# Performance work log

Hardware: AMD Instinct MI355X
Metric: run time of the kernel (lower is better)

## Reference

```python
import jax, jax.numpy as jnp
import numpy as np

B, S, F, D, H, L, NSUB, DFF = 64, 128, 62, 256, 4, 6, 32, 512
DH = D // 2           # each attention branch works on half of d_model
DEPTH = DH // H       # per-head dim = 32
NEG = -1000000000.0


def _rescale(w):
    # (1+e) / (1+exp(1-w))
    e1 = jnp.exp(jnp.float32(1.0))
    return (1.0 + e1) / (1.0 + jnp.exp(1.0 - w))


def _ln(x, g, b):
    mu = jnp.mean(x, -1, keepdims=True)
    v = jnp.var(x, -1, keepdims=True)
    return (x - mu) / jnp.sqrt(v + 1e-6) * g + b


def _heads(x, W, b):
    bsz, s, _ = x.shape
    return (x @ W + b).reshape(bsz, s, H, DEPTH).transpose(0, 2, 1, 3)  # (B,H,S,depth)


def setup_inputs():
    key = jax.random.key(0)
    ks = list(jax.random.split(key, 16))
    it = iter(ks)
    n = lambda shape: jax.random.normal(next(it), shape, jnp.float32) * 0.02
    inp = {
        "x": jax.random.normal(next(it), (B, S, F), jnp.float32),
        "adj_matrix": jax.random.normal(next(it), (B, S, S), jnp.float32),
        "dist_matrix": jax.random.uniform(next(it), (B, S, S), jnp.float32) * 10.0,
        "atom_match_matrix": jax.random.uniform(next(it), (B, NSUB, S), jnp.float32),
        "sum_atoms": jnp.ones((B, NSUB, 1), jnp.float32),
        "emb_W": n((F, D)), "emb_b": jnp.zeros((D,), jnp.float32),
        "glob_W": n((D, D)), "glob_b": jnp.zeros((D,), jnp.float32),
    }
    # per-layer params, stacked along leading L axis for lax.scan
    for p in ["Wq1", "Wk1", "Wv1", "Wo1", "Wq2", "Wk2", "Wv2", "Wo2"]:
        inp[p] = n((L, DH, DH))
    for p in ["bq1", "bk1", "bv1", "bo1", "bq2", "bk2", "bv2", "bo2"]:
        inp[p] = jnp.zeros((L, DH), jnp.float32)
    inp["Wf1"] = n((L, D, DFF)); inp["bf1"] = jnp.zeros((L, DFF), jnp.float32)
    inp["Wf2"] = n((L, DFF, D)); inp["bf2"] = jnp.zeros((L, D), jnp.float32)
    inp["g1"] = jnp.ones((L, D), jnp.float32); inp["be1"] = jnp.zeros((L, D), jnp.float32)
    inp["g2"] = jnp.ones((L, D), jnp.float32); inp["be2"] = jnp.zeros((L, D), jnp.float32)
    return inp


def reference(x, adj_matrix, dist_matrix, atom_match_matrix, sum_atoms,
              emb_W, emb_b, glob_W, glob_b,
              Wq1, Wk1, Wv1, Wo1, Wq2, Wk2, Wv2, Wo2,
              bq1, bk1, bv1, bo1, bq2, bk2, bv2, bo2,
              Wf1, bf1, Wf2, bf2, g1, be1, g2, be2):
    # padding mask from raw atom features: (B,1,1,S)
    mask = (jnp.sum(x, -1) == 0).astype(jnp.float32)[:, None, None, :]
    adj = adj_matrix[:, None]                  # (B,1,S,S) additive bias
    dist = _rescale(dist_matrix)[:, None]      # (B,1,S,S) multiplicative bias
    scale = 1.0 / jnp.sqrt(jnp.float32(DEPTH))

    h = jax.nn.relu(x @ emb_W + emb_b)         # embedding (eval mode, no dropout)

    def layer(h, p):
        (wq1, wk1, wv1, wo1, wq2, wk2, wv2, wo2,
         bq1_, bk1_, bv1_, bo1_, bq2_, bk2_, bv2_, bo2_,
         wf1, bf1_, wf2, bf2_, gg1, bb1, gg2, bb2) = p
        x1, x2 = jnp.split(h, 2, axis=-1)
        # local branch: plain scaled dot product + mask + adjacency bias
        Q = _heads(x1, wq1, bq1_); K = _heads(x1, wk1, bk1_); V = _heads(x1, wv1, bv1_)
        s = jnp.einsum('bhid,bhjd->bhij', Q, K) * scale + mask * NEG + adj
        o = jnp.einsum('bhij,bhjd->bhid', jax.nn.softmax(s, -1), V)
        x_l = o.transpose(0, 2, 1, 3).reshape(h.shape[0], S, DH) @ wo1 + bo1_
        # global branch: relu(QK^T) * rescaled_dist * scale + mask
        Q = _heads(x2, wq2, bq2_); K = _heads(x2, wk2, bk2_); V = _heads(x2, wv2, bv2_)
        s = jax.nn.relu(jnp.einsum('bhid,bhjd->bhij', Q, K)) * dist * scale + mask * NEG
        o = jnp.einsum('bhij,bhjd->bhid', jax.nn.softmax(s, -1), V)
        x_g = o.transpose(0, 2, 1, 3).reshape(h.shape[0], S, DH) @ wo2 + bo2_
        attn = jnp.concatenate([x_l, x_g], -1)
        out1 = _ln(h + attn, gg1, bb1)
        ffn = jax.nn.gelu(out1 @ wf1 + bf1_, approximate=False) @ wf2 + bf2_
        return _ln(ffn + out1, gg2, bb2), None

    xs = (Wq1, Wk1, Wv1, Wo1, Wq2, Wk2, Wv2, Wo2,
          bq1, bk1, bv1, bo1, bq2, bk2, bv2, bo2,
          Wf1, bf1, Wf2, bf2, g1, be1, g2, be2)
    h, _ = jax.lax.scan(layer, h, xs)

    pooled = (atom_match_matrix @ h) / sum_atoms      # (B,NSUB,D)
    out = jax.nn.relu(pooled @ glob_W + glob_b)
    return out
```

## Files before the change

kernel.cpp:

```cpp
#include <hip/hip_runtime.h>
#include <math.h>

#define B_ 64
#define S_ 128
#define F_ 62
#define D_ 256
#define H_ 4
#define L_ 6
#define NSUB_ 32
#define DFF_ 512
#define DH_ 128
#define DEPTH_ 32
#define MS_ (B_*S_)
#define NEGV (-1000000000.0f)
#define SCALE_ 0.17677669529663687f

typedef unsigned short u16;
typedef __attribute__((ext_vector_type(8))) short short8;
typedef __attribute__((ext_vector_type(4))) float f32x4;

__device__ __forceinline__ u16 f2b(float f){
  unsigned u = __float_as_uint(f);
  unsigned r = (u + 0x7fffu + ((u >> 16) & 1u)) >> 16;
  return (u16)r;
}

__device__ __forceinline__ void glds16(const void* g, void* l){
  __builtin_amdgcn_global_load_lds(
      (const __attribute__((address_space(1))) unsigned int*)g,
      (__attribute__((address_space(3))) unsigned int*)l, 16, 0, 0);
}

__global__ __launch_bounds__(256) void adjrescale_kernel(
    const float* __restrict__ adj, const float* __restrict__ dist,
    const float* __restrict__ maskb,
    float* __restrict__ adjm, float* __restrict__ distr){
  size_t i = (size_t)blockIdx.x*256 + threadIdx.x;
  int j = (int)(i & (S_-1));
  int b = (int)(i >> 14);
  const float e1 = 2.718281828459045f;
  distr[i] = (1.0f + e1) / (1.0f + expf(1.0f - dist[i])) * SCALE_;
  adjm[i]  = adj[i] + maskb[b*S_ + j];
}

struct TD { const float* src; u16* dst; int K, N, L; };
struct TDs { TD d[11]; };
__global__ __launch_bounds__(256) void transpose_all_kernel(TDs a){
  const TD p = a.d[blockIdx.z];
  int n0 = blockIdx.x*32, k0 = blockIdx.y*32;
  if(n0 >= p.N || k0 >= p.K) return;
  __shared__ float tbuf[32][33];
  int tx = threadIdx.x, ty = threadIdx.y;
  for(int l = 0; l < p.L; l++){
    const float* src = p.src + (size_t)l*p.K*p.N;
    u16* dst = p.dst + (size_t)l*p.K*p.N;
    #pragma unroll
    for(int i = 0; i < 4; i++)
      tbuf[ty + i*8][tx] = src[(size_t)(k0 + ty + i*8)*p.N + n0 + tx];
    __syncthreads();
    #pragma unroll
    for(int i = 0; i < 4; i++)
      dst[(size_t)(n0 + ty + i*8)*p.K + k0 + tx] = f2b(tbuf[tx][ty + i*8]);
    __syncthreads();
  }
}

__global__ __launch_bounds__(256) void embed_kernel(const float* __restrict__ x,
    const float* __restrict__ W, const float* __restrict__ bias,
    float* __restrict__ h, u16* __restrict__ h_bf, float* __restrict__ maskb){
  __shared__ float xs[4][F_];
  int r0 = blockIdx.x*4;
  int t = threadIdx.x;
  if(t < 4*F_){ int rr = t / F_, ff = t - rr*F_; xs[rr][ff] = x[(size_t)(r0+rr)*F_ + ff]; }
  __syncthreads();
  if(t < 4){
    float s = 0.f;
    #pragma unroll
    for(int f = 0; f < F_; f++) s += xs[t][f];
    maskb[r0 + t] = (s == 0.0f) ? NEGV : 0.0f;
  }
  float b = bias[t];
  float a0=b, a1=b, a2=b, a3=b;
  for(int k=0; k<F_; k++){
    float w = W[k*D_ + t];
    a0 = fmaf(xs[0][k], w, a0);
    a1 = fmaf(xs[1][k], w, a1);
    a2 = fmaf(xs[2][k], w, a2);
    a3 = fmaf(xs[3][k], w, a3);
  }
  a0 = fmaxf(a0, 0.f); a1 = fmaxf(a1, 0.f); a2 = fmaxf(a2, 0.f); a3 = fmaxf(a3, 0.f);
  h[(size_t)(r0+0)*D_ + t] = a0;  h_bf[(size_t)(r0+0)*D_ + t] = f2b(a0);
  h[(size_t)(r0+1)*D_ + t] = a1;  h_bf[(size_t)(r0+1)*D_ + t] = f2b(a1);
  h[(size_t)(r0+2)*D_ + t] = a2;  h_bf[(size_t)(r0+2)*D_ + t] = f2b(a2);
  h[(size_t)(r0+3)*D_ + t] = a3;  h_bf[(size_t)(r0+3)*D_ + t] = f2b(a3);
}

struct MG {
  const u16* A; const u16* W; const float* bias; void* C;
  int lda, K, ldc, aofs, cofs;
};
struct MG6 { MG g[6]; };

template<int TM, bool OUTBF, int ACT>
__global__ __launch_bounds__(256) void mgemm_kernel(MG6 args){
  const MG p = args.g[blockIdx.z];
  __shared__ u16 As[TM*32];
  __shared__ u16 Bs[128*32];
  const int t    = threadIdx.x;
  const int lane = t & 63;
  const int w    = t >> 6;
  const int ln   = lane & 15;
  const int qd   = lane >> 4;
  const int mw   = (w & 1) * (TM/2);
  const int nw   = (w >> 1) * 64;
  const int m0   = blockIdx.x * TM;
  const int n0   = blockIdx.y * 128;
  constexpr int MI = TM/32;
  f32x4 acc[MI][4];
  #pragma unroll
  for(int i=0;i<MI;i++)
    #pragma unroll
    for(int j=0;j<4;j++) acc[i][j] = (f32x4){0.f,0.f,0.f,0.f};

  const int srow = t >> 2;
  const int sc8  = (t & 3) * 8;

  for(int k0 = 0; k0 < p.K; k0 += 32){
    __syncthreads();
    glds16(p.A + (size_t)(m0 + srow)*p.lda + p.aofs + k0 + sc8, As + t*8);
    if(TM == 128)
      glds16(p.A + (size_t)(m0 + 64 + srow)*p.lda + p.aofs + k0 + sc8, As + (t+256)*8);
    glds16(p.W + (size_t)(n0 + srow)*p.K + k0 + sc8, Bs + t*8);
    glds16(p.W + (size_t)(n0 + 64 + srow)*p.K + k0 + sc8, Bs + (t+256)*8);
    __syncthreads();

    short8 a[MI], b[4];
    #pragma unroll
    for(int i=0;i<MI;i++) a[i] = *(const short8*)&As[(mw + i*16 + ln)*32 + qd*8];
    #pragma unroll
    for(int j=0;j<4;j++)  b[j] = *(const short8*)&Bs[(nw + j*16 + ln)*32 + qd*8];
    #pragma unroll
    for(int i=0;i<MI;i++)
      #pragma unroll
      for(int j=0;j<4;j++)
        acc[i][j] = __builtin_amdgcn_mfma_f32_16x16x32_bf16(a[i], b[j], acc[i][j], 0, 0, 0);
  }

  #pragma unroll
  for(int i=0;i<MI;i++){
    #pragma unroll
    for(int j=0;j<4;j++){
      int col = n0 + nw + j*16 + ln;
      float bv = p.bias[col];
      int rowb = m0 + mw + i*16 + qd*4;
      #pragma unroll
      for(int r=0;r<4;r++){
        float v = acc[i][j][r] + bv;
        if(ACT == 1) v = fmaxf(v, 0.f);
        if(ACT == 2) v = 0.5f*v*(1.0f + erff(v*0.70710678118654752f));
        size_t idx = (size_t)(rowb + r)*p.ldc + p.cofs + col;
        if(OUTBF) ((u16*)p.C)[idx] = f2b(v);
        else      ((float*)p.C)[idx] = v;
      }
    }
  }
}

struct QAArgs { const u16 *wq, *wk, *wv; const float *bq, *bk, *bv; };

__global__ __launch_bounds__(256) void qkv_attn_kernel(
    const u16* __restrict__ h_bf,
    QAArgs a1, QAArgs a2,
    const float* __restrict__ adjm, const float* __restrict__ distr,
    const float* __restrict__ maskb,
    u16* __restrict__ o1, u16* __restrict__ o2)
{
  __shared__ u16 SH[21760];
  u16* As = SH;
  u16* Bs = SH + 4096;
  u16* Qs = SH + 7168;
  u16* Ks = SH + 12288;
  u16* Vt = SH + 17408;
  u16* Ps = SH;

  const int bh = blockIdx.x;
  const int b  = bh >> 2;
  const int hh = bh & 3;
  const int branch = blockIdx.y;
  const QAArgs qa = branch ? a2 : a1;
  const u16* wqp = qa.wq + (size_t)hh*32*DH_;
  const u16* wkp = qa.wk + (size_t)hh*32*DH_;
  const u16* wvp = qa.wv + (size_t)hh*32*DH_;
  const int t = threadIdx.x;
  const int w = t >> 6, lane = t & 63;
  const int ln = lane & 15, qd = lane >> 4;
  const size_t rowbase = (size_t)b * S_;
  const int srow = t >> 2, sc8 = (t & 3) * 8;

  f32x4 acc[2][6];
  #pragma unroll
  for(int i=0;i<2;i++)
    #pragma unroll
    for(int j=0;j<6;j++) acc[i][j] = (f32x4){0.f,0.f,0.f,0.f};

  for(int k0 = 0; k0 < DH_; k0 += 32){
    __syncthreads();
    glds16(h_bf + (rowbase + srow)*D_ + branch*DH_ + k0 + sc8, As + t*8);
    glds16(h_bf + (rowbase + 64 + srow)*D_ + branch*DH_ + k0 + sc8, As + (t+256)*8);
    {
      int r = t >> 2;
      const u16* wp = (r < 32) ? wqp : wkp;
      glds16(wp + (size_t)(r & 31)*DH_ + k0 + sc8, Bs + t*8);
    }
    if(t < 128){
      int c = 256 + t;
      glds16(wvp + (size_t)((c>>2) - 64)*DH_ + k0 + (c&3)*8, Bs + c*8);
    }
    __syncthreads();
    short8 av[2];
    #pragma unroll
    for(int mt = 0; mt < 2; mt++)
      av[mt] = *(const short8*)&As[(w*32 + mt*16 + ln)*32 + qd*8];
    #pragma unroll
    for(int nt = 0; nt < 6; nt++){
      short8 bv = *(const short8*)&Bs[(nt*16 + ln)*32 + qd*8];
      #pragma unroll
      for(int mt = 0; mt < 2; mt++)
        acc[mt][nt] = __builtin_amdgcn_mfma_f32_16x16x32_bf16(av[mt], bv, acc[mt][nt], 0, 0, 0);
    }
  }

  {
    const float* bqp = qa.bq + hh*32;
    const float* bkp = qa.bk + hh*32;
    const float* bvp = qa.bv + hh*32;
    #pragma unroll
    for(int mt = 0; mt < 2; mt++){
      int rb = w*32 + mt*16 + qd*4;
      #pragma unroll
      for(int j = 0; j < 2; j++){
        int d = j*16 + ln;
        float bq_ = bqp[d], bk_ = bkp[d], bv_ = bvp[d];
        #pragma unroll
        for(int r = 0; r < 4; r++){
          Qs[(rb+r)*40 + d]   = f2b(acc[mt][j][r]   + bq_);
          Ks[(rb+r)*40 + d]   = f2b(acc[mt][2+j][r] + bk_);
          Vt[d*136 + rb + r]  = f2b(acc[mt][4+j][r] + bv_);
        }
      }
    }
  }
  __syncthreads();

  const int mbase = w * 32;
  short8 qf[2];
  #pragma unroll
  for(int mt = 0; mt < 2; mt++)
    qf[mt] = *(const short8*)&Qs[(mbase + mt*16 + ln)*40 + qd*8];
  short8 kf[8];
  #pragma unroll
  for(int nt = 0; nt < 8; nt++)
    kf[nt] = *(const short8*)&Ks[(nt*16 + ln)*40 + qd*8];
  __syncthreads();

  f32x4 sc[2][8];
  #pragma unroll
  for(int mt = 0; mt < 2; mt++)
    #pragma unroll
    for(int nt = 0; nt < 8; nt++)
      sc[mt][nt] = __builtin_amdgcn_mfma_f32_16x16x32_bf16(
          qf[mt], kf[nt], (f32x4){0.f,0.f,0.f,0.f}, 0, 0, 0);

  float mskv[8];
  if(branch){
    #pragma unroll
    for(int nt = 0; nt < 8; nt++) mskv[nt] = maskb[rowbase + nt*16 + ln];
  }

  #pragma unroll
  for(int mt = 0; mt < 2; mt++){
    #pragma unroll
    for(int r = 0; r < 4; r++){
      int row = mbase + mt*16 + qd*4 + r;
      const float* arow = (branch ? distr : adjm) + (rowbase + row)*S_ + ln;
      #pragma unroll
      for(int nt = 0; nt < 8; nt++){
        float g = arow[nt*16];
        float v;
        if(branch == 0) v = sc[mt][nt][r]*SCALE_ + g;
        else            v = fmaxf(sc[mt][nt][r], 0.f)*g + mskv[nt];
        sc[mt][nt][r] = v;
      }
    }
  }

  #pragma unroll
  for(int mt = 0; mt < 2; mt++){
    #pragma unroll
    for(int r = 0; r < 4; r++){
      float m = -3.4e38f;
      #pragma unroll
      for(int nt = 0; nt < 8; nt++) m = fmaxf(m, sc[mt][nt][r]);
      m = fmaxf(m, __shfl_xor(m, 1));
      m = fmaxf(m, __shfl_xor(m, 2));
      m = fmaxf(m, __shfl_xor(m, 4));
      m = fmaxf(m, __shfl_xor(m, 8));
      float sum = 0.f;
      float e[8];
      #pragma unroll
      for(int nt = 0; nt < 8; nt++){ e[nt] = __expf(sc[mt][nt][r] - m); sum += e[nt]; }
      sum += __shfl_xor(sum, 1);
      sum += __shfl_xor(sum, 2);
      sum += __shfl_xor(sum, 4);
      sum += __shfl_xor(sum, 8);
      float inv = 1.0f / sum;
      int row = mbase + mt*16 + qd*4 + r;
      #pragma unroll
      for(int nt = 0; nt < 8; nt++) Ps[row*136 + nt*16 + ln] = f2b(e[nt] * inv);
    }
  }

  f32x4 oacc[2][2];
  #pragma unroll
  for(int mt = 0; mt < 2; mt++)
    #pragma unroll
    for(int n2 = 0; n2 < 2; n2++) oacc[mt][n2] = (f32x4){0.f,0.f,0.f,0.f};
  #pragma unroll
  for(int kk = 0; kk < 4; kk++){
    short8 pa[2], vb[2];
    #pragma unroll
    for(int mt = 0; mt < 2; mt++)
      pa[mt] = *(const short8*)&Ps[(mbase + mt*16 + ln)*136 + kk*32 + qd*8];
    #pragma unroll
    for(int n2 = 0; n2 < 2; n2++)
      vb[n2] = *(const short8*)&Vt[(n2*16 + ln)*136 + kk*32 + qd*8];
    #pragma unroll
    for(int mt = 0; mt < 2; mt++)
      #pragma unroll
      for(int n2 = 0; n2 < 2; n2++)
        oacc[mt][n2] = __builtin_amdgcn_mfma_f32_16x16x32_bf16(pa[mt], vb[n2], oacc[mt][n2], 0, 0, 0);
  }

  u16* Og = branch ? o2 : o1;
  #pragma unroll
  for(int mt = 0; mt < 2; mt++){
    #pragma unroll
    for(int n2 = 0; n2 < 2; n2++){
      #pragma unroll
      for(int r = 0; r < 4; r++){
        int row = mbase + mt*16 + qd*4 + r;
        int d   = n2*16 + ln;
        Og[(rowbase + row)*DH_ + hh*DEPTH_ + d] = f2b(oacc[mt][n2][r]);
      }
    }
  }
}

struct TailArgs {
  const u16 *o1, *o2, *wo1, *wo2, *w1, *w2;
  const float *bo1, *bo2, *bf1, *bf2, *g1, *be1, *g2, *be2;
  float *h; u16 *h_bf;
};

__global__ __launch_bounds__(256) void tail_kernel(TailArgs p){
  __shared__ u16 X1[32*264];
  __shared__ u16 X2[32*520];
  __shared__ float redS[4][32], redQ[4][32];
  const int t = threadIdx.x;
  const int w = t >> 6, lane = t & 63;
  const int ln = lane & 15, qd = lane >> 4;
  const int m0 = blockIdx.x * 32;
  const int branch = w >> 1;
  const int c0 = w * 64;
  const int bc0 = (w & 1) * 64;

  const u16* Ao = branch ? p.o2 : p.o1;
  const u16* Wo = branch ? p.wo2 : p.wo1;
  const float* bo = branch ? p.bo2 : p.bo1;
  f32x4 y[2][4];
  #pragma unroll
  for(int mt=0;mt<2;mt++)
    #pragma unroll
    for(int nt=0;nt<4;nt++) y[mt][nt] = (f32x4){0.f,0.f,0.f,0.f};

  #pragma unroll
  for(int k0 = 0; k0 < DH_; k0 += 32){
    short8 af[2], bf[4];
    #pragma unroll
    for(int mt=0;mt<2;mt++)
      af[mt] = *(const short8*)(Ao + (size_t)(m0+mt*16+ln)*DH_ + k0 + qd*8);
    #pragma unroll
    for(int nt=0;nt<4;nt++)
      bf[nt] = *(const short8*)(Wo + (size_t)(bc0+nt*16+ln)*DH_ + k0 + qd*8);
    #pragma unroll
    for(int mt=0;mt<2;mt++)
      #pragma unroll
      for(int nt=0;nt<4;nt++)
        y[mt][nt] = __builtin_amdgcn_mfma_f32_16x16x32_bf16(af[mt], bf[nt], y[mt][nt], 0, 0, 0);
  }

  float sS[2][4] = {}, sQ[2][4] = {};
  #pragma unroll
  for(int mt=0;mt<2;mt++){
    #pragma unroll
    for(int nt=0;nt<4;nt++){
      int col = c0 + nt*16 + ln;
      float bv = bo[bc0 + nt*16 + ln];
      #pragma unroll
      for(int r=0;r<4;r++){
        float v = y[mt][nt][r] + bv + p.h[(size_t)(m0+mt*16+qd*4+r)*D_ + col];
        y[mt][nt][r] = v;
        sS[mt][r] += v;
        sQ[mt][r] += v*v;
      }
    }
  }
  #pragma unroll
  for(int mt=0;mt<2;mt++)
    #pragma unroll
    for(int r=0;r<4;r++){
      float a = sS[mt][r], b = sQ[mt][r];
      a += __shfl_xor(a,1); a += __shfl_xor(a,2); a += __shfl_xor(a,4); a += __shfl_xor(a,8);
      b += __shfl_xor(b,1); b += __shfl_xor(b,2); b += __shfl_xor(b,4); b += __shfl_xor(b,8);
      sS[mt][r] = a; sQ[mt][r] = b;
    }
  if(ln == 0){
    #pragma unroll
    for(int mt=0;mt<2;mt++)
      #pragma unroll
      for(int r=0;r<4;r++){
        int row = mt*16 + qd*4 + r;
        redS[w][row] = sS[mt][r];
        redQ[w][row] = sQ[mt][r];
      }
  }
  __syncthreads();
  float mu[2][4], iv[2][4];
  #pragma unroll
  for(int mt=0;mt<2;mt++)
    #pragma unroll
    for(int r=0;r<4;r++){
      int row = mt*16 + qd*4 + r;
      float s = redS[0][row] + redS[1][row] + redS[2][row] + redS[3][row];
      float q = redQ[0][row] + redQ[1][row] + redQ[2][row] + redQ[3][row];
      float m_ = s * (1.0f/D_);
      mu[mt][r] = m_;
      iv[mt][r] = rsqrtf(q*(1.0f/D_) - m_*m_ + 1e-6f);
    }
  #pragma unroll
  for(int mt=0;mt<2;mt++){
    #pragma unroll
    for(int nt=0;nt<4;nt++){
      int col = c0 + nt*16 + ln;
      float gg = p.g1[col], bb = p.be1[col];
      #pragma unroll
      for(int r=0;r<4;r++){
        float yy = (y[mt][nt][r] - mu[mt][r]) * iv[mt][r] * gg + bb;
        y[mt][nt][r] = yy;
        X1[(mt*16+qd*4+r)*264 + col] = f2b(yy);
      }
    }
  }
  __syncthreads();

  {
    const int fc0 = w * 128;
    f32x4 f1[2][8];
    #pragma unroll
    for(int mt=0;mt<2;mt++)
      #pragma unroll
      for(int nt=0;nt<8;nt++) f1[mt][nt] = (f32x4){0.f,0.f,0.f,0.f};
    for(int k0 = 0; k0 < D_; k0 += 32){
      short8 a0 = *(const short8*)&X1[(ln)*264 + k0 + qd*8];
      short8 a1 = *(const short8*)&X1[(16+ln)*264 + k0 + qd*8];
      #pragma unroll
      for(int nt=0;nt<8;nt++){
        short8 bfr = *(const short8*)(p.w1 + (size_t)(fc0+nt*16+ln)*D_ + k0 + qd*8);
        f1[0][nt] = __builtin_amdgcn_mfma_f32_16x16x32_bf16(a0, bfr, f1[0][nt], 0, 0, 0);
        f1[1][nt] = __builtin_amdgcn_mfma_f32_16x16x32_bf16(a1, bfr, f1[1][nt], 0, 0, 0);
      }
    }
    #pragma unroll
    for(int mt=0;mt<2;mt++){
      #pragma unroll
      for(int nt=0;nt<8;nt++){
        int col = fc0 + nt*16 + ln;
        float bv = p.bf1[col];
        #pragma unroll
        for(int r=0;r<4;r++){
          float v = f1[mt][nt][r] + bv;
          v = 0.5f*v*(1.0f + erff(v*0.70710678118654752f));
          X2[(mt*16+qd*4+r)*520 + col] = f2b(v);
        }
      }
    }
  }
  __syncthreads();

  f32x4 f2[2][4];
  #pragma unroll
  for(int mt=0;mt<2;mt++)
    #pragma unroll
    for(int nt=0;nt<4;nt++) f2[mt][nt] = (f32x4){0.f,0.f,0.f,0.f};
  for(int k0 = 0; k0 < DFF_; k0 += 32){
    short8 a0 = *(const short8*)&X2[(ln)*520 + k0 + qd*8];
    short8 a1 = *(const short8*)&X2[(16+ln)*520 + k0 + qd*8];
    #pragma unroll
    for(int nt=0;nt<4;nt++){
      short8 bfr = *(const short8*)(p.w2 + (size_t)(c0+nt*16+ln)*DFF_ + k0 + qd*8);
      f2[0][nt] = __builtin_amdgcn_mfma_f32_16x16x32_bf16(a0, bfr, f2[0][nt], 0, 0, 0);
      f2[1][nt] = __builtin_amdgcn_mfma_f32_16x16x32_bf16(a1, bfr, f2[1][nt], 0, 0, 0);
    }
  }
  float sS2[2][4] = {}, sQ2[2][4] = {};
  #pragma unroll
  for(int mt=0;mt<2;mt++){
    #pragma unroll
    for(int nt=0;nt<4;nt++){
      int col = c0 + nt*16 + ln;
      float bv = p.bf2[col];
      #pragma unroll
      for(int r=0;r<4;r++){
        float v = f2[mt][nt][r] + bv + y[mt][nt][r];
        f2[mt][nt][r] = v;
        sS2[mt][r] += v;
        sQ2[mt][r] += v*v;
      }
    }
  }
  #pragma unroll
  for(int mt=0;mt<2;mt++)
    #pragma unroll
    for(int r=0;r<4;r++){
      float a = sS2[mt][r], b = sQ2[mt][r];
      a += __shfl_xor(a,1); a += __shfl_xor(a,2); a += __shfl_xor(a,4); a += __shfl_xor(a,8);
      b += __shfl_xor(b,1); b += __shfl_xor(b,2); b += __shfl_xor(b,4); b += __shfl_xor(b,8);
      sS2[mt][r] = a; sQ2[mt][r] = b;
    }
  __syncthreads();
  if(ln == 0){
    #pragma unroll
    for(int mt=0;mt<2;mt++)
      #pragma unroll
      for(int r=0;r<4;r++){
        int row = mt*16 + qd*4 + r;
        redS[w][row] = sS2[mt][r];
        redQ[w][row] = sQ2[mt][r];
      }
  }
  __syncthreads();
  #pragma unroll
  for(int mt=0;mt<2;mt++)
    #pragma unroll
    for(int r=0;r<4;r++){
      int row = mt*16 + qd*4 + r;
      float s = redS[0][row] + redS[1][row] + redS[2][row] + redS[3][row];
      float q = redQ[0][row] + redQ[1][row] + redQ[2][row] + redQ[3][row];
      float m_ = s * (1.0f/D_);
      mu[mt][r] = m_;
      iv[mt][r] = rsqrtf(q*(1.0f/D_) - m_*m_ + 1e-6f);
    }
  #pragma unroll
  for(int mt=0;mt<2;mt++){
    #pragma unroll
    for(int nt=0;nt<4;nt++){
      int col = c0 + nt*16 + ln;
      float gg = p.g2[col], bb = p.be2[col];
      #pragma unroll
      for(int r=0;r<4;r++){
        float yy = (f2[mt][nt][r] - mu[mt][r]) * iv[mt][r] * gg + bb;
        size_t idx = (size_t)(m0 + mt*16 + qd*4 + r)*D_ + col;
        p.h[idx] = yy;
        p.h_bf[idx] = f2b(yy);
      }
    }
  }
}

__global__ __launch_bounds__(256) void pool_kernel(
    const float* __restrict__ amm, const float* __restrict__ sum_atoms,
    const float* __restrict__ h, u16* __restrict__ pooled_bf)
{
  __shared__ float as[S_];
  int bn = blockIdx.x;
  int b  = bn >> 5;
  int t  = threadIdx.x;
  if(t < S_) as[t] = amm[(size_t)bn*S_ + t];
  __syncthreads();
  float acc = 0.f;
  const float* hb = h + (size_t)b*S_*D_ + t;
  #pragma unroll 4
  for(int s = 0; s < S_; s++) acc = fmaf(as[s], hb[(size_t)s*D_], acc);
  pooled_bf[(size_t)bn*D_ + t] = f2b(acc / sum_atoms[bn]);
}

extern "C" void kernel_launch(void* const* d_in, const int* in_sizes, int n_in,
                              void* d_out, int out_size, void* d_ws, size_t ws_size,
                              hipStream_t stream)
{
  const float* x     = (const float*)d_in[0];
  const float* adj   = (const float*)d_in[1];
  const float* dist  = (const float*)d_in[2];
  const float* amm   = (const float*)d_in[3];
  const float* sum_a = (const float*)d_in[4];
  const float* embW  = (const float*)d_in[5];
  const float* embB  = (const float*)d_in[6];
  const float* globW = (const float*)d_in[7];
  const float* globB = (const float*)d_in[8];
  const float* Wq1 = (const float*)d_in[9],  *Wk1 = (const float*)d_in[10],
             *Wv1 = (const float*)d_in[11], *Wo1 = (const float*)d_in[12],
             *Wq2 = (const float*)d_in[13], *Wk2 = (const float*)d_in[14],
             *Wv2 = (const float*)d_in[15], *Wo2 = (const float*)d_in[16];
  const float* bq1 = (const float*)d_in[17], *bk1 = (const float*)d_in[18],
             *bv1 = (const float*)d_in[19], *bo1 = (const float*)d_in[20],
             *bq2 = (const float*)d_in[21], *bk2 = (const float*)d_in[22],
             *bv2 = (const float*)d_in[23], *bo2 = (const float*)d_in[24];
  const float* Wf1 = (const float*)d_in[25], *bf1 = (const float*)d_in[26],
             *Wf2 = (const float*)d_in[27], *bf2 = (const float*)d_in[28],
             *g1  = (const float*)d_in[29], *be1 = (const float*)d_in[30],
             *g2  = (const float*)d_in[31], *be2 = (const float*)d_in[32];

  float* wsf = (float*)d_ws;
  float* h     = wsf; wsf += (size_t)MS_*D_;
  float* maskb = wsf; wsf += MS_;
  float* distr = wsf; wsf += (size_t)B_*S_*S_;
  float* adjm  = wsf; wsf += (size_t)B_*S_*S_;
  float* slab  = wsf; wsf += (size_t)MS_*DH_;
  u16* bb = (u16*)wsf;
  u16* h_bf    = bb; bb += (size_t)MS_*D_;
  u16* pooled_bf = bb; bb += (size_t)B_*NSUB_*D_;
  u16* globWt  = bb; bb += (size_t)D_*D_;
  u16* wq1t = bb; bb += (size_t)L_*DH_*DH_;
  u16* wk1t = bb; bb += (size_t)L_*DH_*DH_;
  u16* wv1t = bb; bb += (size_t)L_*DH_*DH_;
  u16* wo1t = bb; bb += (size_t)L_*DH_*DH_;
  u16* wq2t = bb; bb += (size_t)L_*DH_*DH_;
  u16* wk2t = bb; bb += (size_t)L_*DH_*DH_;
  u16* wv2t = bb; bb += (size_t)L_*DH_*DH_;
  u16* wo2t = bb; bb += (size_t)L_*DH_*DH_;
  u16* wf1t = bb; bb += (size_t)L_*D_*DFF_;
  u16* wf2t = bb; bb += (size_t)L_*DFF_*D_;
  u16* o1_bf = (u16*)slab;
  u16* o2_bf = o1_bf + (size_t)MS_*DH_;

  embed_kernel<<<MS_/4, 256, 0, stream>>>(x, embW, embB, h, h_bf, maskb);
  adjrescale_kernel<<<(B_*S_*S_)/256, 256, 0, stream>>>(adj, dist, maskb, adjm, distr);
  {
    TDs td;
    const float* S8[8] = {Wq1, Wk1, Wv1, Wo1, Wq2, Wk2, Wv2, Wo2};
    u16* D8[8] = {wq1t, wk1t, wv1t, wo1t, wq2t, wk2t, wv2t, wo2t};
    for(int i = 0; i < 8; i++) td.d[i] = {S8[i], D8[i], DH_, DH_, L_};
    td.d[8]  = {Wf1, wf1t, D_, DFF_, L_};
    td.d[9]  = {Wf2, wf2t, DFF_, D_, L_};
    td.d[10] = {globW, globWt, D_, D_, 1};
    transpose_all_kernel<<<dim3(16,16,11), dim3(32,8), 0, stream>>>(td);
  }

  for(int l = 0; l < L_; l++){
    QAArgs a1 = { wq1t + (size_t)l*DH_*DH_, wk1t + (size_t)l*DH_*DH_, wv1t + (size_t)l*DH_*DH_,
                  bq1 + (size_t)l*DH_, bk1 + (size_t)l*DH_, bv1 + (size_t)l*DH_ };
    QAArgs a2 = { wq2t + (size_t)l*DH_*DH_, wk2t + (size_t)l*DH_*DH_, wv2t + (size_t)l*DH_*DH_,
                  bq2 + (size_t)l*DH_, bk2 + (size_t)l*DH_, bv2 + (size_t)l*DH_ };
    qkv_attn_kernel<<<dim3(B_*H_, 2), 256, 0, stream>>>(h_bf, a1, a2, adjm, distr, maskb,
                                                        o1_bf, o2_bf);
    TailArgs ta;
    ta.o1 = o1_bf; ta.o2 = o2_bf;
    ta.wo1 = wo1t + (size_t)l*DH_*DH_; ta.wo2 = wo2t + (size_t)l*DH_*DH_;
    ta.w1 = wf1t + (size_t)l*D_*DFF_;  ta.w2 = wf2t + (size_t)l*DFF_*D_;
    ta.bo1 = bo1 + (size_t)l*DH_; ta.bo2 = bo2 + (size_t)l*DH_;
    ta.bf1 = bf1 + (size_t)l*DFF_; ta.bf2 = bf2 + (size_t)l*D_;
    ta.g1 = g1 + (size_t)l*D_; ta.be1 = be1 + (size_t)l*D_;
    ta.g2 = g2 + (size_t)l*D_; ta.be2 = be2 + (size_t)l*D_;
    ta.h = h; ta.h_bf = h_bf;
    tail_kernel<<<MS_/32, 256, 0, stream>>>(ta);
  }

  pool_kernel<<<B_*NSUB_, 256, 0, stream>>>(amm, sum_a, h, pooled_bf);
  {
    MG6 a;
    a.g[0].A = pooled_bf; a.g[0].W = globWt;
    a.g[0].bias = globB; a.g[0].C = (float*)d_out;
    a.g[0].lda = D_; a.g[0].K = D_; a.g[0].ldc = D_;
    a.g[0].aofs = 0; a.g[0].cofs = 0;
    mgemm_kernel<64,false,1><<<dim3((B_*NSUB_)/64, D_/128, 1), 256, 0, stream>>>(a);
  }
}
```

Before: 453.2 us.

## Fuse all layers into persistent mega-kernel with grid barriers and bf16 bias matrices

Replaces the per-layer qkv_attn and tail kernel launches (12 launches) with one persistent kernel of 256 blocks that loops over layers. Software grid barriers built on atomics separate the attention and tail phases. Each block runs two attention units per layer. The adjacency and distance bias matrices are stored as bf16 instead of fp32, which halves their memory traffic, and they are prefetched into registers before the QKV GEMM. The tail FFN is split into two halves so it fits the shared buffer. Risks: the barrier assumes all 256 blocks are co-resident, its spin loop has a timeout, and the bias values lose precision in bf16.

```diff
diff --git a/kernel.cpp b/kernel.cpp
--- a/kernel.cpp
+++ b/kernel.cpp
@@ -24,6 +24,9 @@
   unsigned r = (u + 0x7fffu + ((u >> 16) & 1u)) >> 16;
   return (u16)r;
 }
+__device__ __forceinline__ float b2f(u16 v){
+  return __uint_as_float((unsigned)v << 16);
+}
 
 __device__ __forceinline__ void glds16(const void* g, void* l){
   __builtin_amdgcn_global_load_lds(
@@ -31,16 +34,37 @@
       (__attribute__((address_space(3))) unsigned int*)l, 16, 0, 0);
 }
 
+__device__ __forceinline__ void grid_barrier(unsigned* cnt, unsigned* gen){
+  __syncthreads();
+  if(threadIdx.x == 0){
+    __threadfence_system();
+    unsigned g = __hip_atomic_load(gen, __ATOMIC_RELAXED, __HIP_MEMORY_SCOPE_SYSTEM);
+    unsigned a = __hip_atomic_fetch_add(cnt, 1u, __ATOMIC_ACQ_REL, __HIP_MEMORY_SCOPE_SYSTEM);
+    if(a == gridDim.x - 1u){
+      __hip_atomic_store(cnt, 0u, __ATOMIC_RELAXED, __HIP_MEMORY_SCOPE_SYSTEM);
+      __hip_atomic_store(gen, g + 1u, __ATOMIC_RELEASE, __HIP_MEMORY_SCOPE_SYSTEM);
+    } else {
+      int spins = 0;
+      while(__hip_atomic_load(gen, __ATOMIC_ACQUIRE, __HIP_MEMORY_SCOPE_SYSTEM) == g){
+        __builtin_amdgcn_s_sleep(8);
+        if(++spins > (1 << 20)) break;
+      }
+    }
+    __threadfence_system();
+  }
+  __syncthreads();
+}
+
 __global__ __launch_bounds__(256) void adjrescale_kernel(
     const float* __restrict__ adj, const float* __restrict__ dist,
     const float* __restrict__ maskb,
-    float* __restrict__ adjm, float* __restrict__ distr){
+    u16* __restrict__ adjm16, u16* __restrict__ distr16){
   size_t i = (size_t)blockIdx.x*256 + threadIdx.x;
   int j = (int)(i & (S_-1));
   int b = (int)(i >> 14);
   const float e1 = 2.718281828459045f;
-  distr[i] = (1.0f + e1) / (1.0f + expf(1.0f - dist[i])) * SCALE_;
-  adjm[i]  = adj[i] + maskb[b*S_ + j];
+  distr16[i] = f2b((1.0f + e1) / (1.0f + expf(1.0f - dist[i])) * SCALE_);
+  adjm16[i]  = f2b(adj[i] + maskb[b*S_ + j]);
 }
 
 struct TD { const float* src; u16* dst; int K, N, L; };
@@ -166,16 +190,16 @@
   }
 }
 
-struct QAArgs { const u16 *wq, *wk, *wv; const float *bq, *bk, *bv; };
-
-__global__ __launch_bounds__(256) void qkv_attn_kernel(
-    const u16* __restrict__ h_bf,
-    QAArgs a1, QAArgs a2,
-    const float* __restrict__ adjm, const float* __restrict__ distr,
-    const float* __restrict__ maskb,
-    u16* __restrict__ o1, u16* __restrict__ o2)
-{
-  __shared__ u16 SH[21760];
+struct MegaArgs {
+  float* h; u16* h_bf;
+  u16 *o1, *o2;
+  const u16 *adjm16, *distr16; const float* maskb;
+  const u16 *wq1,*wk1,*wv1,*wo1,*wq2,*wk2,*wv2,*wo2,*wf1,*wf2;
+  const float *bq1,*bk1,*bv1,*bo1,*bq2,*bk2,*bv2,*bo2,*bf1v,*bf2v,*g1,*be1,*g2,*be2;
+  unsigned *cnt, *gen;
+};
+
+__device__ __forceinline__ void qkv_attn_body(u16* SH, int unit, int l, const MegaArgs& p){
   u16* As = SH;
   u16* Bs = SH + 4096;
   u16* Qs = SH + 7168;
@@ -183,19 +207,41 @@
   u16* Vt = SH + 17408;
   u16* Ps = SH;
 
-  const int bh = blockIdx.x;
+  const int branch = unit & 1;
+  const int bh = unit >> 1;
   const int b  = bh >> 2;
   const int hh = bh & 3;
-  const int branch = blockIdx.y;
-  const QAArgs qa = branch ? a2 : a1;
-  const u16* wqp = qa.wq + (size_t)hh*32*DH_;
-  const u16* wkp = qa.wk + (size_t)hh*32*DH_;
-  const u16* wvp = qa.wv + (size_t)hh*32*DH_;
+  const u16* wqp = (branch ? p.wq2 : p.wq1) + (size_t)l*DH_*DH_ + (size_t)hh*32*DH_;
+  const u16* wkp = (branch ? p.wk2 : p.wk1) + (size_t)l*DH_*DH_ + (size_t)hh*32*DH_;
+  const u16* wvp = (branch ? p.wv2 : p.wv1) + (size_t)l*DH_*DH_ + (size_t)hh*32*DH_;
+  const float* bqp = (branch ? p.bq2 : p.bq1) + (size_t)l*DH_ + hh*32;
+  const float* bkp = (branch ? p.bk2 : p.bk1) + (size_t)l*DH_ + hh*32;
+  const float* bvp = (branch ? p.bv2 : p.bv1) + (size_t)l*DH_ + hh*32;
   const int t = threadIdx.x;
   const int w = t >> 6, lane = t & 63;
   const int ln = lane & 15, qd = lane >> 4;
   const size_t rowbase = (size_t)b * S_;
   const int srow = t >> 2, sc8 = (t & 3) * 8;
+  const int mbase = w * 32;
+
+  u16 fixu[2][4][8];
+  {
+    const u16* basep = (branch ? p.distr16 : p.adjm16) + rowbase*S_;
+    #pragma unroll
+    for(int mt = 0; mt < 2; mt++)
+      #pragma unroll
+      for(int r = 0; r < 4; r++){
+        int row = mbase + mt*16 + qd*4 + r;
+        #pragma unroll
+        for(int nt = 0; nt < 8; nt++)
+          fixu[mt][r][nt] = basep[(size_t)row*S_ + nt*16 + ln];
+      }
+  }
+  float mskv[8];
+  if(branch){
+    #pragma unroll
+    for(int nt = 0; nt < 8; nt++) mskv[nt] = p.maskb[rowbase + nt*16 + ln];
+  }
 
   f32x4 acc[2][6];
   #pragma unroll
@@ -205,8 +251,8 @@
 
   for(int k0 = 0; k0 < DH_; k0 += 32){
     __syncthreads();
-    glds16(h_bf + (rowbase + srow)*D_ + branch*DH_ + k0 + sc8, As + t*8);
-    glds16(h_bf + (rowbase + 64 + srow)*D_ + branch*DH_ + k0 + sc8, As + (t+256)*8);
+    glds16(p.h_bf + (rowbase + srow)*D_ + branch*DH_ + k0 + sc8, As + t*8);
+    glds16(p.h_bf + (rowbase + 64 + srow)*D_ + branch*DH_ + k0 + sc8, As + (t+256)*8);
     {
       int r = t >> 2;
       const u16* wp = (r < 32) ? wqp : wkp;
@@ -230,29 +276,23 @@
     }
   }
 
-  {
-    const float* bqp = qa.bq + hh*32;
-    const float* bkp = qa.bk + hh*32;
-    const float* bvp = qa.bv + hh*32;
-    #pragma unroll
-    for(int mt = 0; mt < 2; mt++){
-      int rb = w*32 + mt*16 + qd*4;
-      #pragma unroll
-      for(int j = 0; j < 2; j++){
-        int d = j*16 + ln;
-        float bq_ = bqp[d], bk_ = bkp[d], bv_ = bvp[d];
-        #pragma unroll
-        for(int r = 0; r < 4; r++){
-          Qs[(rb+r)*40 + d]   = f2b(acc[mt][j][r]   + bq_);
-          Ks[(rb+r)*40 + d]   = f2b(acc[mt][2+j][r] + bk_);
-          Vt[d*136 + rb + r]  = f2b(acc[mt][4+j][r] + bv_);
-        }
-      }
-    }
-  }
-  __syncthreads();
-
-  const int mbase = w * 32;
+  #pragma unroll
+  for(int mt = 0; mt < 2; mt++){
+    int rb = w*32 + mt*16 + qd*4;
+    #pragma unroll
+    for(int j = 0; j < 2; j++){
+      int d = j*16 + ln;
+      float bq_ = bqp[d], bk_ = bkp[d], bv_ = bvp[d];
+      #pragma unroll
+      for(int r = 0; r < 4; r++){
+        Qs[(rb+r)*40 + d]   = f2b(acc[mt][j][r]   + bq_);
+        Ks[(rb+r)*40 + d]   = f2b(acc[mt][2+j][r] + bk_);
+        Vt[d*136 + rb + r]  = f2b(acc[mt][4+j][r] + bv_);
+      }
+    }
+  }
+  __syncthreads();
+
   short8 qf[2];
   #pragma unroll
   for(int mt = 0; mt < 2; mt++)
@@ -271,21 +311,13 @@
       sc[mt][nt] = __builtin_amdgcn_mfma_f32_16x16x32_bf16(
           qf[mt], kf[nt], (f32x4){0.f,0.f,0.f,0.f}, 0, 0, 0);
 
-  float mskv[8];
-  if(branch){
-    #pragma unroll
-    for(int nt = 0; nt < 8; nt++) mskv[nt] = maskb[rowbase + nt*16 + ln];
-  }
-
   #pragma unroll
   for(int mt = 0; mt < 2; mt++){
     #pragma unroll
     for(int r = 0; r < 4; r++){
-      int row = mbase + mt*16 + qd*4 + r;
-      const float* arow = (branch ? distr : adjm) + (rowbase + row)*S_ + ln;
       #pragma unroll
       for(int nt = 0; nt < 8; nt++){
-        float g = arow[nt*16];
+        float g = b2f(fixu[mt][r][nt]);
         float v;
         if(branch == 0) v = sc[mt][nt][r]*SCALE_ + g;
         else            v = fmaxf(sc[mt][nt][r], 0.f)*g + mskv[nt];
@@ -341,7 +373,7 @@
         oacc[mt][n2] = __builtin_amdgcn_mfma_f32_16x16x32_bf16(pa[mt], vb[n2], oacc[mt][n2], 0, 0, 0);
   }
 
-  u16* Og = branch ? o2 : o1;
+  u16* Og = branch ? p.o2 : p.o1;
   #pragma unroll
   for(int mt = 0; mt < 2; mt++){
     #pragma unroll
@@ -356,49 +388,49 @@
   }
 }
 
-struct TailArgs {
-  const u16 *o1, *o2, *wo1, *wo2, *w1, *w2;
-  const float *bo1, *bo2, *bf1, *bf2, *g1, *be1, *g2, *be2;
-  float *h; u16 *h_bf;
-};
-
-__global__ __launch_bounds__(256) void tail_kernel(TailArgs p){
-  __shared__ u16 X1[32*264];
-  __shared__ u16 X2[32*520];
-  __shared__ float redS[4][32], redQ[4][32];
+__device__ __forceinline__ void tail_body(u16* SH, int m0, int l, const MegaArgs& p){
+  u16* X1 = SH;
+  u16* X2 = SH + 8448;
+  float* redS = (float*)(SH + 16896);
+  float* redQ = redS + 128;
   const int t = threadIdx.x;
   const int w = t >> 6, lane = t & 63;
   const int ln = lane & 15, qd = lane >> 4;
-  const int m0 = blockIdx.x * 32;
   const int branch = w >> 1;
   const int c0 = w * 64;
   const int bc0 = (w & 1) * 64;
-
   const u16* Ao = branch ? p.o2 : p.o1;
-  const u16* Wo = branch ? p.wo2 : p.wo1;
-  const float* bo = branch ? p.bo2 : p.bo1;
+  const u16* Wo = (branch ? p.wo2 : p.wo1) + (size_t)l*DH_*DH_;
+  const float* bo = (branch ? p.bo2 : p.bo1) + (size_t)l*DH_;
+  const u16* w1 = p.wf1 + (size_t)l*D_*DFF_;
+  const u16* w2 = p.wf2 + (size_t)l*DFF_*D_;
+  const float* bfv1 = p.bf1v + (size_t)l*DFF_;
+  const float* bfv2 = p.bf2v + (size_t)l*D_;
+  const float* g1v = p.g1 + (size_t)l*D_;
+  const float* be1v = p.be1 + (size_t)l*D_;
+  const float* g2v = p.g2 + (size_t)l*D_;
+  const float* be2v = p.be2 + (size_t)l*D_;
+
   f32x4 y[2][4];
   #pragma unroll
   for(int mt=0;mt<2;mt++)
     #pragma unroll
     for(int nt=0;nt<4;nt++) y[mt][nt] = (f32x4){0.f,0.f,0.f,0.f};
-
   #pragma unroll
   for(int k0 = 0; k0 < DH_; k0 += 32){
-    short8 af[2], bf[4];
+    short8 af[2], bfr[4];
     #pragma unroll
     for(int mt=0;mt<2;mt++)
       af[mt] = *(const short8*)(Ao + (size_t)(m0+mt*16+ln)*DH_ + k0 + qd*8);
     #pragma unroll
     for(int nt=0;nt<4;nt++)
-      bf[nt] = *(const short8*)(Wo + (size_t)(bc0+nt*16+ln)*DH_ + k0 + qd*8);
+      bfr[nt] = *(const short8*)(Wo + (size_t)(bc0+nt*16+ln)*DH_ + k0 + qd*8);
     #pragma unroll
     for(int mt=0;mt<2;mt++)
       #pragma unroll
       for(int nt=0;nt<4;nt++)
-        y[mt][nt] = __builtin_amdgcn_mfma_f32_16x16x32_bf16(af[mt], bf[nt], y[mt][nt], 0, 0, 0);
-  }
-
+        y[mt][nt] = __builtin_amdgcn_mfma_f32_16x16x32_bf16(af[mt], bfr[nt], y[mt][nt], 0, 0, 0);
+  }
   float sS[2][4] = {}, sQ[2][4] = {};
   #pragma unroll
   for(int mt=0;mt<2;mt++){
@@ -410,8 +442,7 @@
       for(int r=0;r<4;r++){
         float v = y[mt][nt][r] + bv + p.h[(size_t)(m0+mt*16+qd*4+r)*D_ + col];
         y[mt][nt][r] = v;
-        sS[mt][r] += v;
-        sQ[mt][r] += v*v;
+        sS[mt][r] += v; sQ[mt][r] += v*v;
       }
     }
   }
@@ -419,10 +450,10 @@
   for(int mt=0;mt<2;mt++)
     #pragma unroll
     for(int r=0;r<4;r++){
-      float a = sS[mt][r], b = sQ[mt][r];
+      float a = sS[mt][r], bq = sQ[mt][r];
       a += __shfl_xor(a,1); a += __shfl_xor(a,2); a += __shfl_xor(a,4); a += __shfl_xor(a,8);
-      b += __shfl_xor(b,1); b += __shfl_xor(b,2); b += __shfl_xor(b,4); b += __shfl_xor(b,8);
-      sS[mt][r] = a; sQ[mt][r] = b;
+      bq += __shfl_xor(bq,1); bq += __shfl_xor(bq,2); bq += __shfl_xor(bq,4); bq += __shfl_xor(bq,8);
+      sS[mt][r] = a; sQ[mt][r] = bq;
     }
   if(ln == 0){
     #pragma unroll
@@ -430,8 +461,8 @@
       #pragma unroll
       for(int r=0;r<4;r++){
         int row = mt*16 + qd*4 + r;
-        redS[w][row] = sS[mt][r];
-        redQ[w][row] = sQ[mt][r];
+        redS[w*32 + row] = sS[mt][r];
+        redQ[w*32 + row] = sQ[mt][r];
       }
   }
   __syncthreads();
@@ -441,8 +472,8 @@
     #pragma unroll
     for(int r=0;r<4;r++){
       int row = mt*16 + qd*4 + r;
-      float s = redS[0][row] + redS[1][row] + redS[2][row] + redS[3][row];
-      float q = redQ[0][row] + redQ[1][row] + redQ[2][row] + redQ[3][row];
+      float s = redS[row] + redS[32+row] + redS[64+row] + redS[96+row];
+      float q = redQ[row] + redQ[32+row] + redQ[64+row] + redQ[96+row];
       float m_ = s * (1.0f/D_);
       mu[mt][r] = m_;
       iv[mt][r] = rsqrtf(q*(1.0f/D_) - m_*m_ + 1e-6f);
@@ -452,7 +483,7 @@
     #pragma unroll
     for(int nt=0;nt<4;nt++){
       int col = c0 + nt*16 + ln;
-      float gg = p.g1[col], bb = p.be1[col];
+      float gg = g1v[col], bb = be1v[col];
       #pragma unroll
       for(int r=0;r<4;r++){
         float yy = (y[mt][nt][r] - mu[mt][r]) * iv[mt][r] * gg + bb;
@@ -463,19 +494,24 @@
   }
   __syncthreads();
 
-  {
-    const int fc0 = w * 128;
-    f32x4 f1[2][8];
+  f32x4 f2a[2][4];
+  #pragma unroll
+  for(int mt=0;mt<2;mt++)
+    #pragma unroll
+    for(int nt=0;nt<4;nt++) f2a[mt][nt] = (f32x4){0.f,0.f,0.f,0.f};
+
+  for(int hf = 0; hf < 2; hf++){
+    f32x4 f1[2][4];
     #pragma unroll
     for(int mt=0;mt<2;mt++)
       #pragma unroll
-      for(int nt=0;nt<8;nt++) f1[mt][nt] = (f32x4){0.f,0.f,0.f,0.f};
+      for(int nt=0;nt<4;nt++) f1[mt][nt] = (f32x4){0.f,0.f,0.f,0.f};
     for(int k0 = 0; k0 < D_; k0 += 32){
-      short8 a0 = *(const short8*)&X1[(ln)*264 + k0 + qd*8];
+      short8 a0 = *(const short8*)&X1[ln*264 + k0 + qd*8];
       short8 a1 = *(const short8*)&X1[(16+ln)*264 + k0 + qd*8];
       #pragma unroll
-      for(int nt=0;nt<8;nt++){
-        short8 bfr = *(const short8*)(p.w1 + (size_t)(fc0+nt*16+ln)*D_ + k0 + qd*8);
+      for(int nt=0;nt<4;nt++){
+        short8 bfr = *(const short8*)(w1 + (size_t)(hf*256 + w*64 + nt*16+ln)*D_ + k0 + qd*8);
         f1[0][nt] = __builtin_amdgcn_mfma_f32_16x16x32_bf16(a0, bfr, f1[0][nt], 0, 0, 0);
         f1[1][nt] = __builtin_amdgcn_mfma_f32_16x16x32_bf16(a1, bfr, f1[1][nt], 0, 0, 0);
       }
@@ -483,48 +519,43 @@
     #pragma unroll
     for(int mt=0;mt<2;mt++){
       #pragma unroll
-      for(int nt=0;nt<8;nt++){
-        int col = fc0 + nt*16 + ln;
-        float bv = p.bf1[col];
+      for(int nt=0;nt<4;nt++){
+        int lcol = w*64 + nt*16 + ln;
+        float bv = bfv1[hf*256 + lcol];
         #pragma unroll
         for(int r=0;r<4;r++){
           float v = f1[mt][nt][r] + bv;
           v = 0.5f*v*(1.0f + erff(v*0.70710678118654752f));
-          X2[(mt*16+qd*4+r)*520 + col] = f2b(v);
+          X2[(mt*16+qd*4+r)*264 + lcol] = f2b(v);
         }
       }
     }
-  }
-  __syncthreads();
-
-  f32x4 f2[2][4];
-  #pragma unroll
-  for(int mt=0;mt<2;mt++)
-    #pragma unroll
-    for(int nt=0;nt<4;nt++) f2[mt][nt] = (f32x4){0.f,0.f,0.f,0.f};
-  for(int k0 = 0; k0 < DFF_; k0 += 32){
-    short8 a0 = *(const short8*)&X2[(ln)*520 + k0 + qd*8];
-    short8 a1 = *(const short8*)&X2[(16+ln)*520 + k0 + qd*8];
-    #pragma unroll
-    for(int nt=0;nt<4;nt++){
-      short8 bfr = *(const short8*)(p.w2 + (size_t)(c0+nt*16+ln)*DFF_ + k0 + qd*8);
-      f2[0][nt] = __builtin_amdgcn_mfma_f32_16x16x32_bf16(a0, bfr, f2[0][nt], 0, 0, 0);
-      f2[1][nt] = __builtin_amdgcn_mfma_f32_16x16x32_bf16(a1, bfr, f2[1][nt], 0, 0, 0);
-    }
-  }
+    __syncthreads();
+    for(int k0 = 0; k0 < 256; k0 += 32){
+      short8 a0 = *(const short8*)&X2[ln*264 + k0 + qd*8];
+      short8 a1 = *(const short8*)&X2[(16+ln)*264 + k0 + qd*8];
+      #pragma unroll
+      for(int nt=0;nt<4;nt++){
+        short8 bfr = *(const short8*)(w2 + (size_t)(c0+nt*16+ln)*DFF_ + hf*256 + k0 + qd*8);
+        f2a[0][nt] = __builtin_amdgcn_mfma_f32_16x16x32_bf16(a0, bfr, f2a[0][nt], 0, 0, 0);
+        f2a[1][nt] = __builtin_amdgcn_mfma_f32_16x16x32_bf16(a1, bfr, f2a[1][nt], 0, 0, 0);
+      }
+    }
+    __syncthreads();
+  }
+
   float sS2[2][4] = {}, sQ2[2][4] = {};
   #pragma unroll
   for(int mt=0;mt<2;mt++){
     #pragma unroll
     for(int nt=0;nt<4;nt++){
       int col = c0 + nt*16 + ln;
-      float bv = p.bf2[col];
+      float bv = bfv2[col];
       #pragma unroll
       for(int r=0;r<4;r++){
-        float v = f2[mt][nt][r] + bv + y[mt][nt][r];
-        f2[mt][nt][r] = v;
-        sS2[mt][r] += v;
-        sQ2[mt][r] += v*v;
+        float v = f2a[mt][nt][r] + bv + y[mt][nt][r];
+        f2a[mt][nt][r] = v;
+        sS2[mt][r] += v; sQ2[mt][r] += v*v;
       }
     }
   }
@@ -532,20 +563,19 @@
   for(int mt=0;mt<2;mt++)
     #pragma unroll
     for(int r=0;r<4;r++){
-      float a = sS2[mt][r], b = sQ2[mt][r];
+      float a = sS2[mt][r], bq = sQ2[mt][r];
       a += __shfl_xor(a,1); a += __shfl_xor(a,2); a += __shfl_xor(a,4); a += __shfl_xor(a,8);
-      b += __shfl_xor(b,1); b += __shfl_xor(b,2); b += __shfl_xor(b,4); b += __shfl_xor(b,8);
-      sS2[mt][r] = a; sQ2[mt][r] = b;
-    }
-  __syncthreads();
+      bq += __shfl_xor(bq,1); bq += __shfl_xor(bq,2); bq += __shfl_xor(bq,4); bq += __shfl_xor(bq,8);
+      sS2[mt][r] = a; sQ2[mt][r] = bq;
+    }
   if(ln == 0){
     #pragma unroll
     for(int mt=0;mt<2;mt++)
       #pragma unroll
       for(int r=0;r<4;r++){
         int row = mt*16 + qd*4 + r;
-        redS[w][row] = sS2[mt][r];
-        redQ[w][row] = sQ2[mt][r];
+        redS[w*32 + row] = sS2[mt][r];
+        redQ[w*32 + row] = sQ2[mt][r];
       }
   }
   __syncthreads();
@@ -554,8 +584,8 @@
     #pragma unroll
     for(int r=0;r<4;r++){
       int row = mt*16 + qd*4 + r;
-      float s = redS[0][row] + redS[1][row] + redS[2][row] + redS[3][row];
-      float q = redQ[0][row] + redQ[1][row] + redQ[2][row] + redQ[3][row];
+      float s = redS[row] + redS[32+row] + redS[64+row] + redS[96+row];
+      float q = redQ[row] + redQ[32+row] + redQ[64+row] + redQ[96+row];
       float m_ = s * (1.0f/D_);
       mu[mt][r] = m_;
       iv[mt][r] = rsqrtf(q*(1.0f/D_) - m_*m_ + 1e-6f);
@@ -565,15 +595,27 @@
     #pragma unroll
     for(int nt=0;nt<4;nt++){
       int col = c0 + nt*16 + ln;
-      float gg = p.g2[col], bb = p.be2[col];
+      float gg = g2v[col], bb = be2v[col];
       #pragma unroll
       for(int r=0;r<4;r++){
-        float yy = (f2[mt][nt][r] - mu[mt][r]) * iv[mt][r] * gg + bb;
+        float yy = (f2a[mt][nt][r] - mu[mt][r]) * iv[mt][r] * gg + bb;
         size_t idx = (size_t)(m0 + mt*16 + qd*4 + r)*D_ + col;
         p.h[idx] = yy;
         p.h_bf[idx] = f2b(yy);
       }
     }
+  }
+}
+
+__global__ __launch_bounds__(256, 1) void mega_kernel(MegaArgs p){
+  __shared__ u16 SH[21760];
+  for(int l = 0; l < L_; l++){
+    qkv_attn_body(SH, 2*blockIdx.x + 0, l, p);
+    __syncthreads();
+    qkv_attn_body(SH, 2*blockIdx.x + 1, l, p);
+    grid_barrier(p.cnt, p.gen);
+    tail_body(SH, blockIdx.x*32, l, p);
+    if(l < L_-1) grid_barrier(p.cnt, p.gen);
   }
 }
 
@@ -623,10 +665,12 @@
   float* wsf = (float*)d_ws;
   float* h     = wsf; wsf += (size_t)MS_*D_;
   float* maskb = wsf; wsf += MS_;
-  float* distr = wsf; wsf += (size_t)B_*S_*S_;
-  float* adjm  = wsf; wsf += (size_t)B_*S_*S_;
-  float* slab  = wsf; wsf += (size_t)MS_*DH_;
+  unsigned* barrier = (unsigned*)wsf; wsf += 64;
   u16* bb = (u16*)wsf;
+  u16* adjm16  = bb; bb += (size_t)B_*S_*S_;
+  u16* distr16 = bb; bb += (size_t)B_*S_*S_;
+  u16* o1_bf   = bb; bb += (size_t)MS_*DH_;
+  u16* o2_bf   = bb; bb += (size_t)MS_*DH_;
   u16* h_bf    = bb; bb += (size_t)MS_*D_;
   u16* pooled_bf = bb; bb += (size_t)B_*NSUB_*D_;
   u16* globWt  = bb; bb += (size_t)D_*D_;
@@ -640,11 +684,10 @@
   u16* wo2t = bb; bb += (size_t)L_*DH_*DH_;
   u16* wf1t = bb; bb += (size_t)L_*D_*DFF_;
   u16* wf2t = bb; bb += (size_t)L_*DFF_*D_;
-  u16* o1_bf = (u16*)slab;
-  u16* o2_bf = o1_bf + (size_t)MS_*DH_;
-
+
+  hipMemsetAsync(barrier, 0, 16, stream);
   embed_kernel<<<MS_/4, 256, 0, stream>>>(x, embW, embB, h, h_bf, maskb);
-  adjrescale_kernel<<<(B_*S_*S_)/256, 256, 0, stream>>>(adj, dist, maskb, adjm, distr);
+  adjrescale_kernel<<<(B_*S_*S_)/256, 256, 0, stream>>>(adj, dist, maskb, adjm16, distr16);
   {
     TDs td;
     const float* S8[8] = {Wq1, Wk1, Wv1, Wo1, Wq2, Wk2, Wv2, Wo2};
@@ -656,24 +699,19 @@
     transpose_all_kernel<<<dim3(16,16,11), dim3(32,8), 0, stream>>>(td);
   }
 
-  for(int l = 0; l < L_; l++){
-    QAArgs a1 = { wq1t + (size_t)l*DH_*DH_, wk1t + (size_t)l*DH_*DH_, wv1t + (size_t)l*DH_*DH_,
-                  bq1 + (size_t)l*DH_, bk1 + (size_t)l*DH_, bv1 + (size_t)l*DH_ };
-    QAArgs a2 = { wq2t + (size_t)l*DH_*DH_, wk2t + (size_t)l*DH_*DH_, wv2t + (size_t)l*DH_*DH_,
-                  bq2 + (size_t)l*DH_, bk2 + (size_t)l*DH_, bv2 + (size_t)l*DH_ };
-    qkv_attn_kernel<<<dim3(B_*H_, 2), 256, 0, stream>>>(h_bf, a1, a2, adjm, distr, maskb,
-                                                        o1_bf, o2_bf);
-    TailArgs ta;
-    ta.o1 = o1_bf; ta.o2 = o2_bf;
-    ta.wo1 = wo1t + (size_t)l*DH_*DH_; ta.wo2 = wo2t + (size_t)l*DH_*DH_;
-    ta.w1 = wf1t + (size_t)l*D_*DFF_;  ta.w2 = wf2t + (size_t)l*DFF_*D_;
-    ta.bo1 = bo1 + (size_t)l*DH_; ta.bo2 = bo2 + (size_t)l*DH_;
-    ta.bf1 = bf1 + (size_t)l*DFF_; ta.bf2 = bf2 + (size_t)l*D_;
-    ta.g1 = g1 + (size_t)l*D_; ta.be1 = be1 + (size_t)l*D_;
-    ta.g2 = g2 + (size_t)l*D_; ta.be2 = be2 + (size_t)l*D_;
-    ta.h = h; ta.h_bf = h_bf;
-    tail_kernel<<<MS_/32, 256, 0, stream>>>(ta);
-  }
+  MegaArgs ma;
+  ma.h = h; ma.h_bf = h_bf;
+  ma.o1 = o1_bf; ma.o2 = o2_bf;
+  ma.adjm16 = adjm16; ma.distr16 = distr16; ma.maskb = maskb;
+  ma.wq1 = wq1t; ma.wk1 = wk1t; ma.wv1 = wv1t; ma.wo1 = wo1t;
+  ma.wq2 = wq2t; ma.wk2 = wk2t; ma.wv2 = wv2t; ma.wo2 = wo2t;
+  ma.wf1 = wf1t; ma.wf2 = wf2t;
+  ma.bq1 = bq1; ma.bk1 = bk1; ma.bv1 = bv1; ma.bo1 = bo1;
+  ma.bq2 = bq2; ma.bk2 = bk2; ma.bv2 = bv2; ma.bo2 = bo2;
+  ma.bf1v = bf1; ma.bf2v = bf2;
+  ma.g1 = g1; ma.be1 = be1; ma.g2 = g2; ma.be2 = be2;
+  ma.cnt = barrier; ma.gen = barrier + 1;
+  mega_kernel<<<256, 256, 0, stream>>>(ma);
 
   pool_kernel<<<B_*NSUB_, 256, 0, stream>>>(amm, sum_a, h, pooled_bf);
   {
```

Measured after the change: 965.6 us. 113% more time.
